# Kernel optimization log

Measured on AMD Instinct MI355X. Metric: run time of the kernel, lower is better.

## Reference

```python
import jax, jax.numpy as jnp
import numpy as np

S, D_MODEL, D_INTERNAL = 4096, 2048, 512


def setup_inputs() -> dict:
    key = jax.random.key(0)
    ks = jax.random.split(key, 11)
    sc_in = 1.0 / np.sqrt(D_MODEL)
    return {
        "input_vecs": jax.random.normal(ks[0], (S, D_MODEL), jnp.float32),
        "qw": jax.random.normal(ks[1], (D_INTERNAL, D_MODEL), jnp.float32) * sc_in,
        "qb": jax.random.normal(ks[2], (D_INTERNAL,), jnp.float32) * 0.01,
        "kw": jax.random.normal(ks[3], (D_INTERNAL, D_MODEL), jnp.float32) * sc_in,
        "kb": jax.random.normal(ks[4], (D_INTERNAL,), jnp.float32) * 0.01,
        "vw": jax.random.normal(ks[5], (D_MODEL, D_MODEL), jnp.float32) * sc_in,
        "vb": jax.random.normal(ks[6], (D_MODEL,), jnp.float32) * 0.01,
        "w1": jax.random.normal(ks[7], (D_MODEL, D_MODEL), jnp.float32) * sc_in,
        "b1": jax.random.normal(ks[8], (D_MODEL,), jnp.float32) * 0.01,
        "w2": jax.random.normal(ks[9], (D_MODEL, D_MODEL), jnp.float32) * sc_in,
        "b2": jax.random.normal(ks[10], (D_MODEL,), jnp.float32) * 0.01,
    }


def reference(input_vecs, qw, qb, kw, kb, vw, vb, w1, b1, w2, b2):
    # torch nn.Linear: y = x @ W.T + b
    q = input_vecs @ qw.T + qb              # [S, d_internal]
    k = input_vecs @ kw.T + kb              # [S, d_internal]
    v = input_vecs @ vw.T + vb              # [S, d_model]
    scale = 1.0 / jnp.sqrt(jnp.float32(D_INTERNAL))
    attn = jax.nn.softmax((q @ k.T) * scale, axis=-1)  # [S, S]
    h = attn @ v                            # [S, d_model]
    x_residual = h + input_vecs
    x = jax.nn.relu(x_residual @ w1.T + b1)
    x = x @ w2.T + b2
    hidden = x + x_residual
    return hidden, k, v
```

## Files before the change

kernel.cpp:

```cpp
#include <hip/hip_runtime.h>
#include <cstdint>
#include <cstddef>


typedef __attribute__((ext_vector_type(8))) short short8;
typedef __attribute__((ext_vector_type(4))) float f32x4;

typedef __attribute__((address_space(3))) void lds_void;
typedef __attribute__((address_space(1))) void g_void;

#define SEQ    4096
#define DMODEL 2048
#define DINT   512

#define MEMF() asm volatile("" ::: "memory")
#define BARRIER() do { MEMF(); __builtin_amdgcn_s_barrier(); MEMF(); } while (0)
#define VMCNT12() asm volatile("s_waitcnt vmcnt(12)" ::: "memory")
#define VMCNT6() asm volatile("s_waitcnt vmcnt(6)" ::: "memory")
#define VMCNT0() asm volatile("s_waitcnt vmcnt(0)" ::: "memory")
#define LGKM0()  asm volatile("s_waitcnt lgkmcnt(0)" ::: "memory")

__device__ __forceinline__ unsigned short f2bf(float f) {
  union { float f; unsigned int u; } a;
  a.f = f;
  unsigned int u = a.u;
  u += 0x7fffu + ((u >> 16) & 1u);
  return (unsigned short)(u >> 16);
}
__device__ __forceinline__ float bf2f(unsigned short u) {
  union { unsigned int i; float f; } a;
  a.i = ((unsigned int)u) << 16;
  return a.f;
}

__global__ __launch_bounds__(256) void cast_all_kernel(
    const float* __restrict__ x,  const float* __restrict__ qw,
    const float* __restrict__ kw, const float* __restrict__ vw,
    const float* __restrict__ w1, const float* __restrict__ w2,
    unsigned short* __restrict__ Xb, unsigned short* __restrict__ QKVWb,
    unsigned short* __restrict__ W1b, unsigned short* __restrict__ W2b) {
  const int i = blockIdx.x * 256 + threadIdx.x;
  const float* src; unsigned short* dst; int off;
  if (i < 2097152)      { src = x;  dst = Xb;               off = i; }
  else if (i < 2359296) { src = qw; dst = QKVWb;            off = i - 2097152; }
  else if (i < 2621440) { src = kw; dst = QKVWb + 1048576;  off = i - 2359296; }
  else if (i < 3670016) { src = vw; dst = QKVWb + 2097152;  off = i - 2621440; }
  else if (i < 4718592) { src = w1; dst = W1b;              off = i - 3670016; }
  else                  { src = w2; dst = W2b;              off = i - 4718592; }
  float4 v = ((const float4*)src)[off];
  ushort4 o;
  o.x = f2bf(v.x); o.y = f2bf(v.y); o.z = f2bf(v.z); o.w = f2bf(v.w);
  ((ushort4*)dst)[off] = o;
}

__global__ __launch_bounds__(256)
void gemm_qkv_kernel(const unsigned short* __restrict__ A,
                     const unsigned short* __restrict__ W,
                     int M, int N, int K,
                     const float* __restrict__ qb,
                     const float* __restrict__ kb,
                     const float* __restrict__ vb,
                     float* __restrict__ outK,
                     float* __restrict__ outV,
                     unsigned short* __restrict__ Qb,
                     unsigned short* __restrict__ Kb,
                     unsigned short* __restrict__ VTb)
{
  __shared__ __align__(16) unsigned short As[2][128][32];
  __shared__ __align__(16) unsigned short Bs[2][128][32];

  const int tid  = threadIdx.x;
  const int lane = tid & 63;
  const int wave = tid >> 6;
  const int wr   = wave >> 1;
  const int wc   = wave & 1;
  const int brow = blockIdx.x * 128;
  const int bcol = blockIdx.y * 128;
  const int lr   = lane & 15;
  const int kg   = lane >> 4;

  const int srow  = tid >> 2;
  const int scol  = (tid & 3) * 8;
  const int wbase = wave * 16;
  const unsigned short* Ab = A + (size_t)(brow + srow) * K + scol;
  const unsigned short* Bb = W + (size_t)(bcol + srow) * K + scol;

  f32x4 acc[4][4];
#pragma unroll
  for (int i = 0; i < 4; i++)
#pragma unroll
    for (int j = 0; j < 4; j++) acc[i][j] = (f32x4){0.f, 0.f, 0.f, 0.f};

  auto stage = [&](int d, int k0) {
#pragma unroll
    for (int j = 0; j < 2; ++j) {
      __builtin_amdgcn_global_load_lds((const g_void*)(Ab + (size_t)(j * 64) * K + k0),
                                       (lds_void*)&As[d][j * 64 + wbase][0], 16, 0, 0);
      __builtin_amdgcn_global_load_lds((const g_void*)(Bb + (size_t)(j * 64) * K + k0),
                                       (lds_void*)&Bs[d][j * 64 + wbase][0], 16, 0, 0);
    }
  };

  auto compute = [&](int d) {
    short8 aF[4], bF[4];
#pragma unroll
    for (int mi = 0; mi < 4; ++mi)
      aF[mi] = *(const short8*)&As[d][wr * 64 + mi * 16 + lr][kg * 8];
#pragma unroll
    for (int ni = 0; ni < 4; ++ni)
      bF[ni] = *(const short8*)&Bs[d][wc * 64 + ni * 16 + lr][kg * 8];
#pragma unroll
    for (int mi = 0; mi < 4; ++mi)
#pragma unroll
      for (int ni = 0; ni < 4; ++ni)
        acc[mi][ni] = __builtin_amdgcn_mfma_f32_16x16x32_bf16(
            aF[mi], bF[ni], acc[mi][ni], 0, 0, 0);
  };

  stage(0, 0);
  __syncthreads();
  int c = 0;
  const int NT = K >> 5;
  for (int t = 0; t < NT; ++t) {
    if (t + 1 < NT) stage(c ^ 1, (t + 1) << 5);
    compute(c);
    __syncthreads();
    c ^= 1;
  }

#pragma unroll
  for (int mi = 0; mi < 4; mi++) {
#pragma unroll
    for (int ni = 0; ni < 4; ni++) {
      const int row0 = brow + wr * 64 + mi * 16 + kg * 4;
      const int col  = bcol + wc * 64 + ni * 16 + lr;
      if (col < 512) {
        const float b = qb[col];
#pragma unroll
        for (int r = 0; r < 4; r++)
          Qb[(size_t)(row0 + r) * 512 + col] = f2bf(acc[mi][ni][r] + b);
      } else if (col < 1024) {
        const int c2 = col - 512;
        const float b = kb[c2];
#pragma unroll
        for (int r = 0; r < 4; r++) {
          const float t = acc[mi][ni][r] + b;
          outK[(size_t)(row0 + r) * 512 + c2] = t;
          Kb[(size_t)(row0 + r) * 512 + c2] = f2bf(t);
        }
      } else {
        const int c2 = col - 1024;
        const float b = vb[c2];
        ushort4 o;
#pragma unroll
        for (int r = 0; r < 4; r++) {
          const float t = acc[mi][ni][r] + b;
          outV[(size_t)(row0 + r) * 2048 + c2] = t;
          ((unsigned short*)&o)[r] = f2bf(t);
        }
        *(ushort4*)(&VTb[(size_t)c2 * 4096 + row0]) = o;
      }
    }
  }
}

__global__ __launch_bounds__(512, 2)
void gemm256_kernel(const unsigned short* __restrict__ A,
                    const unsigned short* __restrict__ B,
                    int M, int N, int K,
                    const float* __restrict__ bias,
                    const float* __restrict__ resid,
                    float scale, int relu,
                    float* __restrict__ outF,
                    unsigned short* __restrict__ outB)
{
  __shared__ __align__(16) unsigned short lds[2][2][2][128][64];

  const int tid  = threadIdx.x;
  const int lane = tid & 63;
  const int wave = tid >> 6;
  const int wm   = wave >> 2;
  const int wn   = wave & 3;
  const int lr   = lane & 15;
  const int kg   = lane >> 4;
  const int brow = blockIdx.x * 256;
  const int bcol = blockIdx.y * 256;

  const int srow = tid >> 3;
  const int ssw  = ((tid & 7) * 8) ^ ((srow & 7) << 3);
  const unsigned short* Asrc = A + (size_t)(brow + srow) * K + ssw;
  const unsigned short* Bsrc = B + (size_t)(bcol + srow) * K + ssw;

  char* lbase = (char*)&lds[0][0][0][0][0];
  const int woff = wave * 1024;

  f32x4 acc[8][4];
#pragma unroll
  for (int i = 0; i < 8; ++i)
#pragma unroll
    for (int j = 0; j < 4; ++j) acc[i][j] = (f32x4){0.f, 0.f, 0.f, 0.f};

  const int NT = K >> 6;

  auto SA = [&](int d, int h, int q, int tl) {
    __builtin_amdgcn_global_load_lds(
        (const g_void*)(Asrc + (size_t)(h * 128 + q * 64) * K + tl * 64),
        (lds_void*)(lbase + d * 32768 + h * 16384 + q * 8192 + woff), 16, 0, 0);
  };
  auto SB = [&](int d, int h, int q, int tl) {
    __builtin_amdgcn_global_load_lds(
        (const g_void*)(Bsrc + (size_t)(h * 128 + q * 64) * K + tl * 64),
        (lds_void*)(lbase + 65536 + d * 32768 + h * 16384 + q * 8192 + woff), 16, 0, 0);
  };

  auto LDA = [&](short8* a, int d, int mh, int ks) {
    const char* reg = lbase + d * 32768 + wm * 16384;
    const int ke = (ks * 32 + kg * 8) ^ ((lr & 7) << 3);
#pragma unroll
    for (int i = 0; i < 4; ++i) {
      const int row = (mh * 4 + i) * 16 + lr;
      a[i] = *(const short8*)(reg + row * 128 + ke * 2);
    }
  };
  auto LDB = [&](short8* b, int d, int ks) {
    const char* reg = lbase + 65536 + d * 32768 + (wn >> 1) * 16384;
    const int ke = (ks * 32 + kg * 8) ^ ((lr & 7) << 3);
#pragma unroll
    for (int n = 0; n < 4; ++n) {
      const int row = (wn & 1) * 64 + n * 16 + lr;
      b[n] = *(const short8*)(reg + row * 128 + ke * 2);
    }
  };

  auto MM = [&](int mh, short8* a, short8* b) {
    __builtin_amdgcn_s_setprio(1);
#pragma unroll
    for (int i = 0; i < 4; ++i)
#pragma unroll
      for (int n = 0; n < 4; ++n)
        acc[mh * 4 + i][n] = __builtin_amdgcn_mfma_f32_16x16x32_bf16(
            a[i], b[n], acc[mh * 4 + i][n], 0, 0, 0);
    __builtin_amdgcn_s_setprio(0);
  };

  SA(0, 0, 0, 0); SA(0, 0, 1, 0); SA(0, 1, 0, 0); SA(0, 1, 1, 0);
  SB(0, 0, 0, 0); SB(0, 0, 1, 0); SB(0, 1, 0, 0); SB(0, 1, 1, 0);
  SB(1, 0, 0, 1); SB(1, 0, 1, 1); SA(1, 0, 0, 1);
  SB(1, 1, 0, 1); SB(1, 1, 1, 1); SA(1, 1, 0, 1);
  VMCNT6();
  BARRIER();

  short8 aT[4], bF0[4], bF1[4];
  for (int t = 0; t < NT; ++t) {
    const int buf = t & 1, nb = buf ^ 1;
    const int t1 = (t + 1 < NT) ? t + 1 : NT - 1;
    const int t2 = (t + 2 < NT) ? t + 2 : NT - 1;

    LDA(aT, buf, 0, 0); LDB(bF0, buf, 0);
    SA(nb, 0, 1, t1); SA(nb, 1, 1, t1);
    BARRIER(); MM(0, aT, bF0); BARRIER();

    LDA(aT, buf, 0, 1); LDB(bF1, buf, 1);
    BARRIER(); MM(0, aT, bF1); BARRIER();

    LDA(aT, buf, 1, 0);
    SB(buf, 0, 0, t2); SB(buf, 0, 1, t2); SA(buf, 0, 0, t2);
    BARRIER(); MM(1, aT, bF0); BARRIER();

    LDA(aT, buf, 1, 1);
    SB(buf, 1, 0, t2); SB(buf, 1, 1, t2); SA(buf, 1, 0, t2);
    BARRIER(); MM(1, aT, bF1);
    VMCNT6();
    BARRIER();
  }
  VMCNT0();

#pragma unroll
  for (int mi = 0; mi < 8; ++mi) {
#pragma unroll
    for (int ni = 0; ni < 4; ++ni) {
#pragma unroll
      for (int r = 0; r < 4; ++r) {
        const int row = brow + wm * 128 + mi * 16 + kg * 4 + r;
        const int col = bcol + wn * 64 + ni * 16 + lr;
        float v = acc[mi][ni][r] * scale;
        if (bias)  v += bias[col];
        if (resid) v += resid[(size_t)row * N + col];
        if (relu)  v = fmaxf(v, 0.0f);
        if (outF)  outF[(size_t)row * N + col] = v;
        if (outB)  outB[(size_t)row * N + col] = f2bf(v);
      }
    }
  }
}

__global__ __launch_bounds__(512, 2)
void gemm256x128_k3_kernel(const unsigned short* __restrict__ A,
                           const unsigned short* __restrict__ B,
                           int M, int N, int K,
                           const float* __restrict__ bias,
                           const float* __restrict__ resid,
                           float scale, int relu,
                           float* __restrict__ outF,
                           unsigned short* __restrict__ outB)
{
  __shared__ __align__(16) unsigned short lds[73728];

  const int tid  = threadIdx.x;
  const int lane = tid & 63;
  const int wave = tid >> 6;
  const int wm   = wave >> 1;
  const int wn   = wave & 1;
  const int lr   = lane & 15;
  const int kg   = lane >> 4;
  const int brow = blockIdx.x * 256;
  const int bcol = blockIdx.y * 128;

  const int srow = tid >> 3;
  const int ssw  = ((tid & 7) * 8) ^ ((srow & 7) << 3);
  const unsigned short* Asrc = A + (size_t)(brow + srow) * K + ssw;
  const unsigned short* Bsrc = B + (size_t)(bcol + srow) * K + ssw;

  char* lbase = (char*)&lds[0];
  const int woff = wave * 1024;

  f32x4 acc[4][4];
#pragma unroll
  for (int i = 0; i < 4; ++i)
#pragma unroll
    for (int j = 0; j < 4; ++j) acc[i][j] = (f32x4){0.f, 0.f, 0.f, 0.f};

  const int NT = K >> 6;

  auto STAGE = [&](int d, int tl) {
#pragma unroll
    for (int r = 0; r < 4; ++r)
      __builtin_amdgcn_global_load_lds(
          (const g_void*)(Asrc + (size_t)(r * 64) * K + tl * 64),
          (lds_void*)(lbase + d * 32768 + r * 8192 + woff), 16, 0, 0);
#pragma unroll
    for (int r = 0; r < 2; ++r)
      __builtin_amdgcn_global_load_lds(
          (const g_void*)(Bsrc + (size_t)(r * 64) * K + tl * 64),
          (lds_void*)(lbase + 98304 + d * 16384 + r * 8192 + woff), 16, 0, 0);
  };

  auto RD = [&](short8* a, short8* b, int d) {
#pragma unroll
    for (int ks = 0; ks < 2; ++ks) {
      const int ke = (ks * 32 + kg * 8) ^ ((lr & 7) << 3);
      const char* ra = lbase + d * 32768;
      const char* rb = lbase + 98304 + d * 16384;
#pragma unroll
      for (int mi = 0; mi < 4; ++mi)
        a[ks * 4 + mi] = *(const short8*)(ra + (wm * 64 + mi * 16 + lr) * 128 + ke * 2);
#pragma unroll
      for (int n = 0; n < 4; ++n)
        b[ks * 4 + n] = *(const short8*)(rb + (wn * 64 + n * 16 + lr) * 128 + ke * 2);
    }
  };

  auto MMALL = [&](short8* a, short8* b) {
    __builtin_amdgcn_s_setprio(1);
#pragma unroll
    for (int ks = 0; ks < 2; ++ks)
#pragma unroll
      for (int mi = 0; mi < 4; ++mi)
#pragma unroll
        for (int n = 0; n < 4; ++n)
          acc[mi][n] = __builtin_amdgcn_mfma_f32_16x16x32_bf16(
              a[ks * 4 + mi], b[ks * 4 + n], acc[mi][n], 0, 0, 0);
    __builtin_amdgcn_s_setprio(0);
  };

  STAGE(0, 0);
  STAGE(1, 1);
  STAGE(2, 2);
  VMCNT12();
  BARRIER();
  short8 aE[8], bE[8], aO[8], bO[8];
  RD(aE, bE, 0);
  LGKM0();

  for (int t = 0; t < NT; t += 2) {
    VMCNT6();
    BARRIER();
    STAGE(t % 3, (t + 3 < NT) ? t + 3 : NT - 1);
    RD(aO, bO, (t + 1) % 3);
    MMALL(aE, bE);
    LGKM0();
    VMCNT6();
    BARRIER();
    STAGE((t + 1) % 3, (t + 4 < NT) ? t + 4 : NT - 1);
    RD(aE, bE, (t + 2) % 3);
    MMALL(aO, bO);
    LGKM0();
  }
  VMCNT0();

#pragma unroll
  for (int mi = 0; mi < 4; ++mi) {
#pragma unroll
    for (int ni = 0; ni < 4; ++ni) {
#pragma unroll
      for (int r = 0; r < 4; ++r) {
        const int row = brow + wm * 64 + mi * 16 + kg * 4 + r;
        const int col = bcol + wn * 64 + ni * 16 + lr;
        float v = acc[mi][ni][r] * scale;
        if (bias)  v += bias[col];
        if (resid) v += resid[(size_t)row * N + col];
        if (relu)  v = fmaxf(v, 0.0f);
        if (outF)  outF[(size_t)row * N + col] = v;
        if (outB)  outB[(size_t)row * N + col] = f2bf(v);
      }
    }
  }
}

__global__ __launch_bounds__(256) void softmax_kernel(
    const unsigned short* __restrict__ Scb, unsigned short* __restrict__ P) {
  __shared__ float redm[4];
  __shared__ float reds[4];
  const int tid = threadIdx.x;
  const int row = blockIdx.x;
  const unsigned short* src = Scb + (size_t)row * SEQ;

  short8 h0 = *(const short8*)(src + tid * 8);
  short8 h1 = *(const short8*)(src + tid * 8 + 2048);
  float f[16];
#pragma unroll
  for (int i = 0; i < 8; ++i) f[i]     = bf2f((unsigned short)h0[i]);
#pragma unroll
  for (int i = 0; i < 8; ++i) f[8 + i] = bf2f((unsigned short)h1[i]);

  float lmax = f[0];
#pragma unroll
  for (int i = 1; i < 16; ++i) lmax = fmaxf(lmax, f[i]);
#pragma unroll
  for (int off = 32; off > 0; off >>= 1)
    lmax = fmaxf(lmax, __shfl_xor(lmax, off, 64));
  if ((tid & 63) == 0) redm[tid >> 6] = lmax;
  __syncthreads();
  const float m = fmaxf(fmaxf(redm[0], redm[1]), fmaxf(redm[2], redm[3]));

  float lsum = 0.0f;
#pragma unroll
  for (int i = 0; i < 16; ++i) { f[i] = __expf(f[i] - m); lsum += f[i]; }
#pragma unroll
  for (int off = 32; off > 0; off >>= 1)
    lsum += __shfl_xor(lsum, off, 64);
  if ((tid & 63) == 0) reds[tid >> 6] = lsum;
  __syncthreads();
  const float inv = 1.0f / (reds[0] + reds[1] + reds[2] + reds[3]);

  unsigned short* dst = P + (size_t)row * SEQ;
  short8 o0, o1;
#pragma unroll
  for (int i = 0; i < 8; ++i) o0[i] = (short)f2bf(f[i] * inv);
#pragma unroll
  for (int i = 0; i < 8; ++i) o1[i] = (short)f2bf(f[8 + i] * inv);
  *(short8*)(dst + tid * 8)        = o0;
  *(short8*)(dst + tid * 8 + 2048) = o1;
}

extern "C" void kernel_launch(void* const* d_in, const int* in_sizes, int n_in,
                              void* d_out, int out_size, void* d_ws, size_t ws_size,
                              hipStream_t stream) {
  const float* x  = (const float*)d_in[0];
  const float* qw = (const float*)d_in[1];
  const float* qb = (const float*)d_in[2];
  const float* kw = (const float*)d_in[3];
  const float* kb = (const float*)d_in[4];
  const float* vw = (const float*)d_in[5];
  const float* vb = (const float*)d_in[6];
  const float* w1 = (const float*)d_in[7];
  const float* b1 = (const float*)d_in[8];
  const float* w2 = (const float*)d_in[9];
  const float* b2 = (const float*)d_in[10];
  float* out = (float*)d_out;
  char* ws = (char*)d_ws;

  const size_t MB = 1048576;
  unsigned short* Xb    = (unsigned short*)(ws + 0 * MB);
  unsigned short* QKVWb = (unsigned short*)(ws + 16 * MB);
  unsigned short* Pb    = (unsigned short*)(ws + 0 * MB);
  unsigned short* W1b   = (unsigned short*)(ws + 32 * MB);
  unsigned short* W2b   = (unsigned short*)(ws + 40 * MB);
  unsigned short* Qb    = (unsigned short*)(ws + 48 * MB);
  unsigned short* Kb    = (unsigned short*)(ws + 52 * MB);
  unsigned short* VTb   = (unsigned short*)(ws + 72 * MB);
  unsigned short* Scb   = (unsigned short*)(ws + 88 * MB);
  float*          XR    = (float*)(ws + 88 * MB);
  unsigned short* X1b   = (unsigned short*)(ws + 120 * MB);
  unsigned short* XRb   = (unsigned short*)(ws + 136 * MB);

  cast_all_kernel<<<22528, 256, 0, stream>>>(
      x, qw, kw, vw, w1, w2, Xb, QKVWb, W1b, W2b);

  gemm_qkv_kernel<<<dim3(32, 24), dim3(256), 0, stream>>>(
      Xb, QKVWb, SEQ, 3072, DMODEL, qb, kb, vb,
      out + 8388608, out + 10485760, Qb, Kb, VTb);
  gemm256_kernel<<<dim3(16, 16), dim3(512), 0, stream>>>(
      Qb, Kb, SEQ, SEQ, DINT, nullptr, nullptr,
      0.04419417382415922f, 0, nullptr, Scb);
  softmax_kernel<<<4096, dim3(256), 0, stream>>>(Scb, Pb);
  gemm256x128_k3_kernel<<<dim3(16, 16), dim3(512), 0, stream>>>(
      Pb, VTb, SEQ, DMODEL, SEQ, nullptr, x, 1.0f, 0, XR, XRb);
  gemm256x128_k3_kernel<<<dim3(16, 16), dim3(512), 0, stream>>>(
      XRb, W1b, SEQ, DMODEL, DMODEL, b1, nullptr, 1.0f, 1, nullptr, X1b);
  gemm256x128_k3_kernel<<<dim3(16, 16), dim3(512), 0, stream>>>(
      X1b, W2b, SEQ, DMODEL, DMODEL, b2, XR, 1.0f, 0, out, nullptr);
}
```

Measured before the change: 325.5 us.

## Add 128x128 K32 GEMM for FFN1, drop fp32 residual buffer, slim QK epilogue

New measurement: 314.8 us (median of 2 runs). 1.03x faster.

```diff
diff --git a/kernel.cpp b/kernel.cpp
--- a/kernel.cpp
+++ b/kernel.cpp
@@ -17,6 +17,7 @@
 #define BARRIER() do { MEMF(); __builtin_amdgcn_s_barrier(); MEMF(); } while (0)
 #define VMCNT12() asm volatile("s_waitcnt vmcnt(12)" ::: "memory")
 #define VMCNT6() asm volatile("s_waitcnt vmcnt(6)" ::: "memory")
+#define VMCNT4() asm volatile("s_waitcnt vmcnt(4)" ::: "memory")
 #define VMCNT0() asm volatile("s_waitcnt vmcnt(0)" ::: "memory")
 #define LGKM0()  asm volatile("s_waitcnt lgkmcnt(0)" ::: "memory")
 
@@ -168,11 +169,7 @@
 void gemm256_kernel(const unsigned short* __restrict__ A,
                     const unsigned short* __restrict__ B,
                     int M, int N, int K,
-                    const float* __restrict__ bias,
-                    const float* __restrict__ resid,
-                    float scale, int relu,
-                    float* __restrict__ outF,
-                    unsigned short* __restrict__ outB)
+                    float scale, unsigned short* __restrict__ outB)
 {
   __shared__ __align__(16) unsigned short lds[2][2][2][128][64];
 
@@ -283,12 +280,7 @@
       for (int r = 0; r < 4; ++r) {
         const int row = brow + wm * 128 + mi * 16 + kg * 4 + r;
         const int col = bcol + wn * 64 + ni * 16 + lr;
-        float v = acc[mi][ni][r] * scale;
-        if (bias)  v += bias[col];
-        if (resid) v += resid[(size_t)row * N + col];
-        if (relu)  v = fmaxf(v, 0.0f);
-        if (outF)  outF[(size_t)row * N + col] = v;
-        if (outB)  outB[(size_t)row * N + col] = f2bf(v);
+        outB[(size_t)row * N + col] = f2bf(acc[mi][ni][r] * scale);
       }
     }
   }
@@ -300,6 +292,7 @@
                            int M, int N, int K,
                            const float* __restrict__ bias,
                            const float* __restrict__ resid,
+                           const unsigned short* __restrict__ residB,
                            float scale, int relu,
                            float* __restrict__ outF,
                            unsigned short* __restrict__ outB)
@@ -407,11 +400,120 @@
         const int row = brow + wm * 64 + mi * 16 + kg * 4 + r;
         const int col = bcol + wn * 64 + ni * 16 + lr;
         float v = acc[mi][ni][r] * scale;
-        if (bias)  v += bias[col];
-        if (resid) v += resid[(size_t)row * N + col];
-        if (relu)  v = fmaxf(v, 0.0f);
-        if (outF)  outF[(size_t)row * N + col] = v;
-        if (outB)  outB[(size_t)row * N + col] = f2bf(v);
+        if (bias)   v += bias[col];
+        if (resid)  v += resid[(size_t)row * N + col];
+        if (residB) v += bf2f(residB[(size_t)row * N + col]);
+        if (relu)   v = fmaxf(v, 0.0f);
+        if (outF)   outF[(size_t)row * N + col] = v;
+        if (outB)   outB[(size_t)row * N + col] = f2bf(v);
+      }
+    }
+  }
+}
+
+__global__ __launch_bounds__(256, 2)
+void gemm_k32_kernel(const unsigned short* __restrict__ A,
+                     const unsigned short* __restrict__ B,
+                     int M, int N, int K,
+                     const float* __restrict__ bias, int relu,
+                     unsigned short* __restrict__ outB)
+{
+  __shared__ __align__(16) unsigned short lds[24576];
+
+  const int tid  = threadIdx.x;
+  const int lane = tid & 63;
+  const int wave = tid >> 6;
+  const int wr   = wave >> 1;
+  const int wc   = wave & 1;
+  const int lr   = lane & 15;
+  const int kg   = lane >> 4;
+  const int brow = blockIdx.x * 128;
+  const int bcol = blockIdx.y * 128;
+
+  const int srow = tid >> 2;
+  const int ssw  = ((tid & 3) * 8) ^ ((srow & 3) << 3);
+  const unsigned short* Asrc = A + (size_t)(brow + srow) * K + ssw;
+  const unsigned short* Bsrc = B + (size_t)(bcol + srow) * K + ssw;
+
+  char* lbase = (char*)&lds[0];
+  const int woff = wave * 1024;
+
+  f32x4 acc[4][4];
+#pragma unroll
+  for (int i = 0; i < 4; ++i)
+#pragma unroll
+    for (int j = 0; j < 4; ++j) acc[i][j] = (f32x4){0.f, 0.f, 0.f, 0.f};
+
+  const int NT = K >> 5;
+
+  auto STAGE = [&](int d, int tl) {
+#pragma unroll
+    for (int r = 0; r < 2; ++r)
+      __builtin_amdgcn_global_load_lds(
+          (const g_void*)(Asrc + (size_t)(r * 64) * K + tl * 32),
+          (lds_void*)(lbase + d * 8192 + r * 4096 + woff), 16, 0, 0);
+#pragma unroll
+    for (int r = 0; r < 2; ++r)
+      __builtin_amdgcn_global_load_lds(
+          (const g_void*)(Bsrc + (size_t)(r * 64) * K + tl * 32),
+          (lds_void*)(lbase + 24576 + d * 8192 + r * 4096 + woff), 16, 0, 0);
+  };
+
+  auto RD = [&](short8* a, short8* b, int d) {
+#pragma unroll
+    for (int mi = 0; mi < 4; ++mi) {
+      const int row = wr * 64 + mi * 16 + lr;
+      a[mi] = *(const short8*)(lbase + d * 8192 + row * 64 + ((kg ^ (row & 3)) << 4));
+    }
+#pragma unroll
+    for (int n = 0; n < 4; ++n) {
+      const int row = wc * 64 + n * 16 + lr;
+      b[n] = *(const short8*)(lbase + 24576 + d * 8192 + row * 64 + ((kg ^ (row & 3)) << 4));
+    }
+  };
+
+  auto MM = [&](short8* a, short8* b) {
+    __builtin_amdgcn_s_setprio(1);
+#pragma unroll
+    for (int mi = 0; mi < 4; ++mi)
+#pragma unroll
+      for (int n = 0; n < 4; ++n)
+        acc[mi][n] = __builtin_amdgcn_mfma_f32_16x16x32_bf16(
+            a[mi], b[n], acc[mi][n], 0, 0, 0);
+    __builtin_amdgcn_s_setprio(0);
+  };
+
+  STAGE(0, 0);
+  STAGE(1, 1);
+  VMCNT4();
+  BARRIER();
+
+  short8 aF[4], bF[4];
+  int cur = 0, stg = 2;
+  for (int t = 0; t < NT; ++t) {
+    VMCNT4();
+    BARRIER();
+    STAGE(stg, (t + 2 < NT) ? t + 2 : NT - 1);
+    RD(aF, bF, cur);
+    MM(aF, bF);
+    LGKM0();
+    cur = (cur == 2) ? 0 : cur + 1;
+    stg = (stg == 2) ? 0 : stg + 1;
+  }
+  VMCNT0();
+
+#pragma unroll
+  for (int mi = 0; mi < 4; ++mi) {
+#pragma unroll
+    for (int ni = 0; ni < 4; ++ni) {
+#pragma unroll
+      for (int r = 0; r < 4; ++r) {
+        const int row = brow + wr * 64 + mi * 16 + kg * 4 + r;
+        const int col = bcol + wc * 64 + ni * 16 + lr;
+        float v = acc[mi][ni][r];
+        if (bias) v += bias[col];
+        if (relu) v = fmaxf(v, 0.0f);
+        outB[(size_t)row * N + col] = f2bf(v);
       }
     }
   }
@@ -490,7 +592,6 @@
   unsigned short* Kb    = (unsigned short*)(ws + 52 * MB);
   unsigned short* VTb   = (unsigned short*)(ws + 72 * MB);
   unsigned short* Scb   = (unsigned short*)(ws + 88 * MB);
-  float*          XR    = (float*)(ws + 88 * MB);
   unsigned short* X1b   = (unsigned short*)(ws + 120 * MB);
   unsigned short* XRb   = (unsigned short*)(ws + 136 * MB);
 
@@ -501,13 +602,12 @@
       Xb, QKVWb, SEQ, 3072, DMODEL, qb, kb, vb,
       out + 8388608, out + 10485760, Qb, Kb, VTb);
   gemm256_kernel<<<dim3(16, 16), dim3(512), 0, stream>>>(
-      Qb, Kb, SEQ, SEQ, DINT, nullptr, nullptr,
-      0.04419417382415922f, 0, nullptr, Scb);
+      Qb, Kb, SEQ, SEQ, DINT, 0.04419417382415922f, Scb);
   softmax_kernel<<<4096, dim3(256), 0, stream>>>(Scb, Pb);
   gemm256x128_k3_kernel<<<dim3(16, 16), dim3(512), 0, stream>>>(
-      Pb, VTb, SEQ, DMODEL, SEQ, nullptr, x, 1.0f, 0, XR, XRb);
+      Pb, VTb, SEQ, DMODEL, SEQ, nullptr, x, nullptr, 1.0f, 0, nullptr, XRb);
+  gemm_k32_kernel<<<dim3(32, 16), dim3(256), 0, stream>>>(
+      XRb, W1b, SEQ, DMODEL, DMODEL, b1, 1, X1b);
   gemm256x128_k3_kernel<<<dim3(16, 16), dim3(512), 0, stream>>>(
-      XRb, W1b, SEQ, DMODEL, DMODEL, b1, nullptr, 1.0f, 1, nullptr, X1b);
-  gemm256x128_k3_kernel<<<dim3(16, 16), dim3(512), 0, stream>>>(
-      X1b, W2b, SEQ, DMODEL, DMODEL, b2, XR, 1.0f, 0, out, nullptr);
-}
+      X1b, W2b, SEQ, DMODEL, DMODEL, b2, nullptr, XRb, 1.0f, 0, out, nullptr);
+}
```

## Replace 256x128 GEMMs with 128x128 K32 triple-buffered kernel and bf16 residual

Applied to the files above, without the earlier changes.

Result: slower. 340.7 us (+4.7%).

```diff
diff --git a/kernel.cpp b/kernel.cpp
--- a/kernel.cpp
+++ b/kernel.cpp
@@ -15,8 +15,8 @@
 
 #define MEMF() asm volatile("" ::: "memory")
 #define BARRIER() do { MEMF(); __builtin_amdgcn_s_barrier(); MEMF(); } while (0)
-#define VMCNT12() asm volatile("s_waitcnt vmcnt(12)" ::: "memory")
 #define VMCNT6() asm volatile("s_waitcnt vmcnt(6)" ::: "memory")
+#define VMCNT4() asm volatile("s_waitcnt vmcnt(4)" ::: "memory")
 #define VMCNT0() asm volatile("s_waitcnt vmcnt(0)" ::: "memory")
 #define LGKM0()  asm volatile("s_waitcnt lgkmcnt(0)" ::: "memory")
 
@@ -53,85 +53,135 @@
   ((ushort4*)dst)[off] = o;
 }
 
-__global__ __launch_bounds__(256)
-void gemm_qkv_kernel(const unsigned short* __restrict__ A,
-                     const unsigned short* __restrict__ W,
+
+#define K32_DECLS \
+  const int tid  = threadIdx.x;                                             \
+  const int lane = tid & 63;                                                \
+  const int wave = tid >> 6;                                                \
+  const int wr   = wave >> 1;                                               \
+  const int wc   = wave & 1;                                                \
+  const int lr   = lane & 15;                                               \
+  const int kg   = lane >> 4;                                               \
+  const int brow = blockIdx.x * 128;                                        \
+  const int bcol = blockIdx.y * 128;                                        \
+  const int srow = tid >> 2;                                                \
+  const int ssw  = ((tid & 3) * 8) ^ ((srow & 3) << 3);                     \
+  const unsigned short* Asrc = A + (size_t)(brow + srow) * K + ssw;         \
+  const unsigned short* Bsrc = B + (size_t)(bcol + srow) * K + ssw;         \
+  char* lbase = (char*)&lds[0];                                             \
+  const int woff = wave * 1024;                                             \
+  f32x4 acc[4][4];                                                          \
+  _Pragma("unroll") for (int i = 0; i < 4; ++i)                             \
+    _Pragma("unroll") for (int j = 0; j < 4; ++j)                           \
+      acc[i][j] = (f32x4){0.f, 0.f, 0.f, 0.f};                              \
+  auto STAGE = [&](int d, int tl) {                                         \
+    _Pragma("unroll") for (int r = 0; r < 2; ++r)                           \
+      __builtin_amdgcn_global_load_lds(                                     \
+          (const g_void*)(Asrc + (size_t)(r * 64) * K + tl * 32),           \
+          (lds_void*)(lbase + d * 8192 + r * 4096 + woff), 16, 0, 0);       \
+    _Pragma("unroll") for (int r = 0; r < 2; ++r)                           \
+      __builtin_amdgcn_global_load_lds(                                     \
+          (const g_void*)(Bsrc + (size_t)(r * 64) * K + tl * 32),           \
+          (lds_void*)(lbase + 24576 + d * 8192 + r * 4096 + woff), 16, 0, 0); \
+  };                                                                        \
+  auto RD = [&](short8* a, short8* b, int d) {                              \
+    _Pragma("unroll") for (int mi = 0; mi < 4; ++mi) {                      \
+      const int row = wr * 64 + mi * 16 + lr;                               \
+      a[mi] = *(const short8*)(lbase + d * 8192 + row * 64 +                \
+                               ((kg ^ (row & 3)) << 4));                    \
+    }                                                                       \
+    _Pragma("unroll") for (int n = 0; n < 4; ++n) {                         \
+      const int row = wc * 64 + n * 16 + lr;                                \
+      b[n] = *(const short8*)(lbase + 24576 + d * 8192 + row * 64 +         \
+                              ((kg ^ (row & 3)) << 4));                     \
+    }                                                                       \
+  };                                                                        \
+  auto MM = [&](short8* a, short8* b) {                                     \
+    __builtin_amdgcn_s_setprio(1);                                          \
+    _Pragma("unroll") for (int mi = 0; mi < 4; ++mi)                        \
+      _Pragma("unroll") for (int n = 0; n < 4; ++n)                         \
+        acc[mi][n] = __builtin_amdgcn_mfma_f32_16x16x32_bf16(               \
+            a[mi], b[n], acc[mi][n], 0, 0, 0);                              \
+    __builtin_amdgcn_s_setprio(0);                                          \
+  }
+
+#define K32_LOOP \
+  STAGE(0, 0);                                                              \
+  STAGE(1, 1);                                                              \
+  VMCNT4();                                                                 \
+  BARRIER();                                                                \
+  short8 aF[4], bF[4];                                                      \
+  int cur = 0, stg = 2;                                                     \
+  for (int t = 0; t < NT; ++t) {                                            \
+    VMCNT4();                                                               \
+    BARRIER();                                                              \
+    STAGE(stg, (t + 2 < NT) ? t + 2 : NT - 1);                              \
+    RD(aF, bF, cur);                                                        \
+    MM(aF, bF);                                                             \
+    LGKM0();                                                                \
+    cur = (cur == 2) ? 0 : cur + 1;                                         \
+    stg = (stg == 2) ? 0 : stg + 1;                                         \
+  }                                                                         \
+  VMCNT0()
+
+__global__ __launch_bounds__(256, 2)
+void gemm_k32_kernel(const unsigned short* __restrict__ A,
+                     const unsigned short* __restrict__ B,
                      int M, int N, int K,
-                     const float* __restrict__ qb,
-                     const float* __restrict__ kb,
-                     const float* __restrict__ vb,
-                     float* __restrict__ outK,
-                     float* __restrict__ outV,
-                     unsigned short* __restrict__ Qb,
-                     unsigned short* __restrict__ Kb,
-                     unsigned short* __restrict__ VTb)
+                     const float* __restrict__ bias,
+                     const float* __restrict__ residF,
+                     const unsigned short* __restrict__ residB,
+                     int relu,
+                     float* __restrict__ outF,
+                     unsigned short* __restrict__ outB)
 {
-  __shared__ __align__(16) unsigned short As[2][128][32];
-  __shared__ __align__(16) unsigned short Bs[2][128][32];
-
-  const int tid  = threadIdx.x;
-  const int lane = tid & 63;
-  const int wave = tid >> 6;
-  const int wr   = wave >> 1;
-  const int wc   = wave & 1;
-  const int brow = blockIdx.x * 128;
-  const int bcol = blockIdx.y * 128;
-  const int lr   = lane & 15;
-  const int kg   = lane >> 4;
-
-  const int srow  = tid >> 2;
-  const int scol  = (tid & 3) * 8;
-  const int wbase = wave * 16;
-  const unsigned short* Ab = A + (size_t)(brow + srow) * K + scol;
-  const unsigned short* Bb = W + (size_t)(bcol + srow) * K + scol;
-
-  f32x4 acc[4][4];
-#pragma unroll
-  for (int i = 0; i < 4; i++)
-#pragma unroll
-    for (int j = 0; j < 4; j++) acc[i][j] = (f32x4){0.f, 0.f, 0.f, 0.f};
-
-  auto stage = [&](int d, int k0) {
-#pragma unroll
-    for (int j = 0; j < 2; ++j) {
-      __builtin_amdgcn_global_load_lds((const g_void*)(Ab + (size_t)(j * 64) * K + k0),
-                                       (lds_void*)&As[d][j * 64 + wbase][0], 16, 0, 0);
-      __builtin_amdgcn_global_load_lds((const g_void*)(Bb + (size_t)(j * 64) * K + k0),
-                                       (lds_void*)&Bs[d][j * 64 + wbase][0], 16, 0, 0);
+  __shared__ __align__(16) unsigned short lds[24576];
+  K32_DECLS;
+  const int NT = K >> 5;
+  K32_LOOP;
+
+#pragma unroll
+  for (int mi = 0; mi < 4; ++mi) {
+#pragma unroll
+    for (int ni = 0; ni < 4; ++ni) {
+#pragma unroll
+      for (int r = 0; r < 4; ++r) {
+        const int row = brow + wr * 64 + mi * 16 + kg * 4 + r;
+        const int col = bcol + wc * 64 + ni * 16 + lr;
+        float v = acc[mi][ni][r];
+        if (bias)   v += bias[col];
+        if (residF) v += residF[(size_t)row * N + col];
+        if (residB) v += bf2f(residB[(size_t)row * N + col]);
+        if (relu)   v = fmaxf(v, 0.0f);
+        if (outF)   outF[(size_t)row * N + col] = v;
+        if (outB)   outB[(size_t)row * N + col] = f2bf(v);
+      }
     }
-  };
-
-  auto compute = [&](int d) {
-    short8 aF[4], bF[4];
-#pragma unroll
-    for (int mi = 0; mi < 4; ++mi)
-      aF[mi] = *(const short8*)&As[d][wr * 64 + mi * 16 + lr][kg * 8];
-#pragma unroll
-    for (int ni = 0; ni < 4; ++ni)
-      bF[ni] = *(const short8*)&Bs[d][wc * 64 + ni * 16 + lr][kg * 8];
-#pragma unroll
-    for (int mi = 0; mi < 4; ++mi)
-#pragma unroll
-      for (int ni = 0; ni < 4; ++ni)
-        acc[mi][ni] = __builtin_amdgcn_mfma_f32_16x16x32_bf16(
-            aF[mi], bF[ni], acc[mi][ni], 0, 0, 0);
-  };
-
-  stage(0, 0);
-  __syncthreads();
-  int c = 0;
+  }
+}
+
+__global__ __launch_bounds__(256, 2)
+void gemm_qkv_k32_kernel(const unsigned short* __restrict__ A,
+                         const unsigned short* __restrict__ B,
+                         int M, int N, int K,
+                         const float* __restrict__ qb,
+                         const float* __restrict__ kb,
+                         const float* __restrict__ vb,
+                         float* __restrict__ outK,
+                         float* __restrict__ outV,
+                         unsigned short* __restrict__ Qb,
+                         unsigned short* __restrict__ Kb,
+                         unsigned short* __restrict__ VTb)
+{
+  __shared__ __align__(16) unsigned short lds[24576];
+  K32_DECLS;
   const int NT = K >> 5;
-  for (int t = 0; t < NT; ++t) {
-    if (t + 1 < NT) stage(c ^ 1, (t + 1) << 5);
-    compute(c);
-    __syncthreads();
-    c ^= 1;
-  }
-
-#pragma unroll
-  for (int mi = 0; mi < 4; mi++) {
-#pragma unroll
-    for (int ni = 0; ni < 4; ni++) {
+  K32_LOOP;
+
+#pragma unroll
+  for (int mi = 0; mi < 4; ++mi) {
+#pragma unroll
+    for (int ni = 0; ni < 4; ++ni) {
       const int row0 = brow + wr * 64 + mi * 16 + kg * 4;
       const int col  = bcol + wc * 64 + ni * 16 + lr;
       if (col < 512) {
@@ -168,11 +218,7 @@
 void gemm256_kernel(const unsigned short* __restrict__ A,
                     const unsigned short* __restrict__ B,
                     int M, int N, int K,
-                    const float* __restrict__ bias,
-                    const float* __restrict__ resid,
-                    float scale, int relu,
-                    float* __restrict__ outF,
-                    unsigned short* __restrict__ outB)
+                    float scale, unsigned short* __restrict__ outB)
 {
   __shared__ __align__(16) unsigned short lds[2][2][2][128][64];
 
@@ -283,135 +329,7 @@
       for (int r = 0; r < 4; ++r) {
         const int row = brow + wm * 128 + mi * 16 + kg * 4 + r;
         const int col = bcol + wn * 64 + ni * 16 + lr;
-        float v = acc[mi][ni][r] * scale;
-        if (bias)  v += bias[col];
-        if (resid) v += resid[(size_t)row * N + col];
-        if (relu)  v = fmaxf(v, 0.0f);
-        if (outF)  outF[(size_t)row * N + col] = v;
-        if (outB)  outB[(size_t)row * N + col] = f2bf(v);
-      }
-    }
-  }
-}
-
-__global__ __launch_bounds__(512, 2)
-void gemm256x128_k3_kernel(const unsigned short* __restrict__ A,
-                           const unsigned short* __restrict__ B,
-                           int M, int N, int K,
-                           const float* __restrict__ bias,
-                           const float* __restrict__ resid,
-                           float scale, int relu,
-                           float* __restrict__ outF,
-                           unsigned short* __restrict__ outB)
-{
-  __shared__ __align__(16) unsigned short lds[73728];
-
-  const int tid  = threadIdx.x;
-  const int lane = tid & 63;
-  const int wave = tid >> 6;
-  const int wm   = wave >> 1;
-  const int wn   = wave & 1;
-  const int lr   = lane & 15;
-  const int kg   = lane >> 4;
-  const int brow = blockIdx.x * 256;
-  const int bcol = blockIdx.y * 128;
-
-  const int srow = tid >> 3;
-  const int ssw  = ((tid & 7) * 8) ^ ((srow & 7) << 3);
-  const unsigned short* Asrc = A + (size_t)(brow + srow) * K + ssw;
-  const unsigned short* Bsrc = B + (size_t)(bcol + srow) * K + ssw;
-
-  char* lbase = (char*)&lds[0];
-  const int woff = wave * 1024;
-
-  f32x4 acc[4][4];
-#pragma unroll
-  for (int i = 0; i < 4; ++i)
-#pragma unroll
-    for (int j = 0; j < 4; ++j) acc[i][j] = (f32x4){0.f, 0.f, 0.f, 0.f};
-
-  const int NT = K >> 6;
-
-  auto STAGE = [&](int d, int tl) {
-#pragma unroll
-    for (int r = 0; r < 4; ++r)
-      __builtin_amdgcn_global_load_lds(
-          (const g_void*)(Asrc + (size_t)(r * 64) * K + tl * 64),
-          (lds_void*)(lbase + d * 32768 + r * 8192 + woff), 16, 0, 0);
-#pragma unroll
-    for (int r = 0; r < 2; ++r)
-      __builtin_amdgcn_global_load_lds(
-          (const g_void*)(Bsrc + (size_t)(r * 64) * K + tl * 64),
-          (lds_void*)(lbase + 98304 + d * 16384 + r * 8192 + woff), 16, 0, 0);
-  };
-
-  auto RD = [&](short8* a, short8* b, int d) {
-#pragma unroll
-    for (int ks = 0; ks < 2; ++ks) {
-      const int ke = (ks * 32 + kg * 8) ^ ((lr & 7) << 3);
-      const char* ra = lbase + d * 32768;
-      const char* rb = lbase + 98304 + d * 16384;
-#pragma unroll
-      for (int mi = 0; mi < 4; ++mi)
-        a[ks * 4 + mi] = *(const short8*)(ra + (wm * 64 + mi * 16 + lr) * 128 + ke * 2);
-#pragma unroll
-      for (int n = 0; n < 4; ++n)
-        b[ks * 4 + n] = *(const short8*)(rb + (wn * 64 + n * 16 + lr) * 128 + ke * 2);
-    }
-  };
-
-  auto MMALL = [&](short8* a, short8* b) {
-    __builtin_amdgcn_s_setprio(1);
-#pragma unroll
-    for (int ks = 0; ks < 2; ++ks)
-#pragma unroll
-      for (int mi = 0; mi < 4; ++mi)
-#pragma unroll
-        for (int n = 0; n < 4; ++n)
-          acc[mi][n] = __builtin_amdgcn_mfma_f32_16x16x32_bf16(
-              a[ks * 4 + mi], b[ks * 4 + n], acc[mi][n], 0, 0, 0);
-    __builtin_amdgcn_s_setprio(0);
-  };
-
-  STAGE(0, 0);
-  STAGE(1, 1);
-  STAGE(2, 2);
-  VMCNT12();
-  BARRIER();
-  short8 aE[8], bE[8], aO[8], bO[8];
-  RD(aE, bE, 0);
-  LGKM0();
-
-  for (int t = 0; t < NT; t += 2) {
-    VMCNT6();
-    BARRIER();
-    STAGE(t % 3, (t + 3 < NT) ? t + 3 : NT - 1);
-    RD(aO, bO, (t + 1) % 3);
-    MMALL(aE, bE);
-    LGKM0();
-    VMCNT6();
-    BARRIER();
-    STAGE((t + 1) % 3, (t + 4 < NT) ? t + 4 : NT - 1);
-    RD(aE, bE, (t + 2) % 3);
-    MMALL(aO, bO);
-    LGKM0();
-  }
-  VMCNT0();
-
-#pragma unroll
-  for (int mi = 0; mi < 4; ++mi) {
-#pragma unroll
-    for (int ni = 0; ni < 4; ++ni) {
-#pragma unroll
-      for (int r = 0; r < 4; ++r) {
-        const int row = brow + wm * 64 + mi * 16 + kg * 4 + r;
-        const int col = bcol + wn * 64 + ni * 16 + lr;
-        float v = acc[mi][ni][r] * scale;
-        if (bias)  v += bias[col];
-        if (resid) v += resid[(size_t)row * N + col];
-        if (relu)  v = fmaxf(v, 0.0f);
-        if (outF)  outF[(size_t)row * N + col] = v;
-        if (outB)  outB[(size_t)row * N + col] = f2bf(v);
+        outB[(size_t)row * N + col] = f2bf(acc[mi][ni][r] * scale);
       }
     }
   }
@@ -490,24 +408,22 @@
   unsigned short* Kb    = (unsigned short*)(ws + 52 * MB);
   unsigned short* VTb   = (unsigned short*)(ws + 72 * MB);
   unsigned short* Scb   = (unsigned short*)(ws + 88 * MB);
-  float*          XR    = (float*)(ws + 88 * MB);
   unsigned short* X1b   = (unsigned short*)(ws + 120 * MB);
   unsigned short* XRb   = (unsigned short*)(ws + 136 * MB);
 
   cast_all_kernel<<<22528, 256, 0, stream>>>(
       x, qw, kw, vw, w1, w2, Xb, QKVWb, W1b, W2b);
 
-  gemm_qkv_kernel<<<dim3(32, 24), dim3(256), 0, stream>>>(
+  gemm_qkv_k32_kernel<<<dim3(32, 24), dim3(256), 0, stream>>>(
       Xb, QKVWb, SEQ, 3072, DMODEL, qb, kb, vb,
       out + 8388608, out + 10485760, Qb, Kb, VTb);
   gemm256_kernel<<<dim3(16, 16), dim3(512), 0, stream>>>(
-      Qb, Kb, SEQ, SEQ, DINT, nullptr, nullptr,
-      0.04419417382415922f, 0, nullptr, Scb);
+      Qb, Kb, SEQ, SEQ, DINT, 0.04419417382415922f, Scb);
   softmax_kernel<<<4096, dim3(256), 0, stream>>>(Scb, Pb);
-  gemm256x128_k3_kernel<<<dim3(16, 16), dim3(512), 0, stream>>>(
-      Pb, VTb, SEQ, DMODEL, SEQ, nullptr, x, 1.0f, 0, XR, XRb);
-  gemm256x128_k3_kernel<<<dim3(16, 16), dim3(512), 0, stream>>>(
-      XRb, W1b, SEQ, DMODEL, DMODEL, b1, nullptr, 1.0f, 1, nullptr, X1b);
-  gemm256x128_k3_kernel<<<dim3(16, 16), dim3(512), 0, stream>>>(
-      X1b, W2b, SEQ, DMODEL, DMODEL, b2, XR, 1.0f, 0, out, nullptr);
-}
+  gemm_k32_kernel<<<dim3(32, 16), dim3(256), 0, stream>>>(
+      Pb, VTb, SEQ, DMODEL, SEQ, nullptr, x, nullptr, 0, nullptr, XRb);
+  gemm_k32_kernel<<<dim3(32, 16), dim3(256), 0, stream>>>(
+      XRb, W1b, SEQ, DMODEL, DMODEL, b1, nullptr, nullptr, 1, nullptr, X1b);
+  gemm_k32_kernel<<<dim3(32, 16), dim3(256), 0, stream>>>(
+      X1b, W2b, SEQ, DMODEL, DMODEL, b2, nullptr, XRb, 0, out, nullptr);
+}
```
